# Performance work log

Hardware: AMD Instinct MI355X
Metric: run time of the kernel (lower is better)

## Reference

```python
import jax, jax.numpy as jnp
import numpy as np

HIDDEN = 1024
FFN = 2048
NUM_EXPERTS = 8
TOP_K = 2
BATCH, SEQ = 2, 1024


def setup_inputs() -> dict:
    key = jax.random.key(0)
    k0, k1, k2, k3, k4 = jax.random.split(key, 5)
    scale = 0.02
    hidden_states = jax.random.normal(k0, (BATCH, SEQ, HIDDEN), dtype=jnp.float32)
    gate_w = jax.random.normal(k1, (NUM_EXPERTS, HIDDEN), dtype=jnp.float32) * scale
    w1 = jax.random.normal(k2, (NUM_EXPERTS, FFN, HIDDEN), dtype=jnp.float32) * scale  # gate proj
    w3 = jax.random.normal(k3, (NUM_EXPERTS, FFN, HIDDEN), dtype=jnp.float32) * scale  # up proj
    w2 = jax.random.normal(k4, (NUM_EXPERTS, HIDDEN, FFN), dtype=jnp.float32) * scale  # down proj
    return {"hidden_states": hidden_states, "gate_w": gate_w, "w1": w1, "w2": w2, "w3": w3}


def reference(hidden_states, gate_w, w1, w2, w3):
    B, S, D = hidden_states.shape
    x = hidden_states.reshape(-1, D)                         # [T, D]
    T = x.shape[0]
    # Router: logits -> fp32 softmax -> top-k -> renormalize
    router_logits = jnp.einsum("td,ed->te", x, gate_w)       # [T, E]
    routing_weights = jax.nn.softmax(router_logits.astype(jnp.float32), axis=1)
    top_vals, top_idx = jax.lax.top_k(routing_weights, TOP_K)  # [T, K]
    top_vals = top_vals / jnp.sum(top_vals, axis=-1, keepdims=True)
    top_vals = top_vals.astype(x.dtype)
    # Per-token-per-expert combine weight (0 for unselected experts)
    w_te = jnp.zeros((T, NUM_EXPERTS), dtype=x.dtype)
    w_te = w_te.at[jnp.arange(T)[:, None], top_idx].add(top_vals)  # [T, E]
    # Fused experts: silu(x W1^T) * (x W3^T) -> W2^T, weighted combine
    g = jax.nn.silu(jnp.einsum("td,efd->tef", x, w1))        # [T, E, F]
    u = jnp.einsum("td,efd->tef", x, w3)                     # [T, E, F]
    y = jnp.einsum("tef,edf->ted", g * u, w2)                # [T, E, D]
    out = jnp.einsum("ted,te->td", y, w_te)                  # [T, D]
    return out.reshape(B, S, D), router_logits
```

## Files before the change

### kernel.cpp

```cpp
#include <hip/hip_runtime.h>
#include <hip/hip_bf16.h>
#include <stdint.h>

#define HIDDEN  1024
#define FFN_DIM 2048
#define NEXP    8
#define NTOK    2048
#define MAXROWS 5120

typedef short bf16x8 __attribute__((ext_vector_type(8)));
typedef float f32x4  __attribute__((ext_vector_type(4)));

static const size_t OFF_CNT  = 0;
static const size_t OFF_BASE = 64;
static const size_t OFF_TOK  = 128;
static const size_t OFF_WGT  = OFF_TOK + (size_t)NEXP*NTOK*4;
static const size_t OFF_XBF  = 131328;
static const size_t XBF_B    = (size_t)NTOK*HIDDEN*2;
static const size_t OFF_W1B  = OFF_XBF + XBF_B;
static const size_t W_B      = (size_t)NEXP*FFN_DIM*HIDDEN*2;
static const size_t OFF_W3B  = OFF_W1B + W_B;
static const size_t OFF_W2B  = OFF_W3B + W_B;
static const size_t OFF_H    = OFF_W2B + W_B;
static const size_t H_B      = (size_t)MAXROWS*FFN_DIM*2;
static const size_t WS_NEED  = OFF_H + H_B;

__device__ __forceinline__ unsigned short f2bf(float f) {
  union { float f; unsigned u; } a; a.f = f;
  unsigned r = a.u + 0x7fff + ((a.u >> 16) & 1);
  return (unsigned short)(r >> 16);
}

__device__ __forceinline__ void ld_g2l16(const void* gsrc, void* ldst) {
  __builtin_amdgcn_global_load_lds(
      (const __attribute__((address_space(1))) unsigned int*)gsrc,
      (__attribute__((address_space(3))) unsigned int*)ldst, 16, 0, 0);
}

__global__ __launch_bounds__(256) void router_kernel(
    const float* __restrict__ x, const float* __restrict__ gw,
    float* __restrict__ logits, int* __restrict__ cnt,
    int* __restrict__ tok, float* __restrict__ wgt)
{
  const int t   = blockIdx.x;
  const int tid = threadIdx.x;
  float4 xv = ((const float4*)(x + (size_t)t * HIDDEN))[tid];
  float p[NEXP];
#pragma unroll
  for (int e = 0; e < NEXP; ++e) {
    float4 gv = ((const float4*)(gw + (size_t)e * HIDDEN))[tid];
    p[e] = xv.x * gv.x + xv.y * gv.y + xv.z * gv.z + xv.w * gv.w;
  }
#pragma unroll
  for (int e = 0; e < NEXP; ++e) {
#pragma unroll
    for (int off = 32; off > 0; off >>= 1)
      p[e] += __shfl_down(p[e], off, 64);
  }
  __shared__ float red[4][NEXP];
  const int wv = tid >> 6, ln = tid & 63;
  if (ln == 0) {
#pragma unroll
    for (int e = 0; e < NEXP; ++e) red[wv][e] = p[e];
  }
  __syncthreads();
  if (tid == 0) {
    float l[NEXP];
#pragma unroll
    for (int e = 0; e < NEXP; ++e) {
      l[e] = red[0][e] + red[1][e] + red[2][e] + red[3][e];
      logits[(size_t)t * NEXP + e] = l[e];
    }
    int i0 = 0;
#pragma unroll
    for (int e = 1; e < NEXP; ++e) if (l[e] > l[i0]) i0 = e;
    int i1 = (i0 == 0) ? 1 : 0;
#pragma unroll
    for (int e = 0; e < NEXP; ++e) if (e != i0 && l[e] > l[i1]) i1 = e;
    float w0 = 1.f / (1.f + expf(l[i1] - l[i0]));
    float w1 = 1.f - w0;
    int s0 = atomicAdd(&cnt[i0], 1);
    tok[i0 * NTOK + s0] = t;  wgt[i0 * NTOK + s0] = w0;
    int s1 = atomicAdd(&cnt[i1], 1);
    tok[i1 * NTOK + s1] = t;  wgt[i1 * NTOK + s1] = w1;
  }
}

__global__ void prefix_kernel(const int* __restrict__ cnt, int* __restrict__ base) {
  if (threadIdx.x == 0 && blockIdx.x == 0) {
    int b = 0;
#pragma unroll
    for (int e = 0; e < NEXP; ++e) { base[e] = b; b += ((cnt[e] + 127) >> 7) << 7; }
    base[NEXP] = b;
  }
}

__global__ __launch_bounds__(256) void cvt_kernel(
    const float* __restrict__ src, unsigned short* __restrict__ dst, int n4)
{
  int i = blockIdx.x * blockDim.x + threadIdx.x;
  const int stride = gridDim.x * blockDim.x;
  for (; i < n4; i += stride) {
    float4 v = ((const float4*)src)[i];
    ushort4 o;
    o.x = f2bf(v.x); o.y = f2bf(v.y); o.z = f2bf(v.z); o.w = f2bf(v.w);
    ((ushort4*)dst)[i] = o;
  }
}

__global__ __launch_bounds__(256) void cvt3_kernel(
    const float* __restrict__ s0, const float* __restrict__ s1, const float* __restrict__ s2,
    unsigned short* __restrict__ d0, unsigned short* __restrict__ d1, unsigned short* __restrict__ d2,
    int n4)
{
  const int start  = blockIdx.x * blockDim.x + threadIdx.x;
  const int stride = gridDim.x * blockDim.x;
#pragma unroll
  for (int pass = 0; pass < 3; ++pass) {
    const float* s = (pass == 0) ? s0 : (pass == 1) ? s1 : s2;
    unsigned short* d = (pass == 0) ? d0 : (pass == 1) ? d1 : d2;
    for (int i = start; i < n4; i += stride) {
      float4 v = ((const float4*)s)[i];
      ushort4 o;
      o.x = f2bf(v.x); o.y = f2bf(v.y); o.z = f2bf(v.z); o.w = f2bf(v.w);
      ((ushort4*)d)[i] = o;
    }
  }
}

__global__ __launch_bounds__(512) void gemm1_kernel(
    const unsigned short* __restrict__ xbf,
    const unsigned short* __restrict__ w1bf,
    const unsigned short* __restrict__ w3bf,
    const int* __restrict__ cnt, const int* __restrict__ base,
    const int* __restrict__ tok,
    unsigned short* __restrict__ H)
{
  const int bid  = blockIdx.x;
  const int e    = bid & 7;
  const int slot = bid >> 3;
  const int mt   = slot & 15;
  const int nt   = slot >> 4;
  const int n = cnt[e];
  if (mt * 128 >= n) return;
  const int t = threadIdx.x;
  const int w = t >> 6, l = t & 63;

  __shared__ unsigned short Xs [128 * 64];
  __shared__ unsigned short W1s[128 * 64];
  __shared__ unsigned short W3s[128 * 64];
  __shared__ int stok[128];

  if (t < 128) {
    int idx = mt * 128 + t;
    stok[t] = tok[e * NTOK + min(idx, n - 1)];
  }
  __syncthreads();

  const int r0 = t >> 3;
  const size_t tok0 = (size_t)stok[r0];
  const size_t tok1 = (size_t)stok[64 + r0];
  const int kp = (((t & 7) ^ ((t >> 3) & 7)) << 3);

  const unsigned short* w1e = w1bf + (size_t)e * FFN_DIM * HIDDEN + (size_t)(nt * 128) * HIDDEN;
  const unsigned short* w3e = w3bf + (size_t)e * FFN_DIM * HIDDEN + (size_t)(nt * 128) * HIDDEN;

  f32x4 acc1[4][2], acc3[4][2];
#pragma unroll
  for (int i = 0; i < 4; ++i)
#pragma unroll
    for (int j = 0; j < 2; ++j) { acc1[i][j] = (f32x4)0.f; acc3[i][j] = (f32x4)0.f; }

  const int Moff = (w & 1) * 64;
  const int Noff = (w >> 1) * 32;
  const int lr = l & 15;
  const int lg = l >> 4;
  char* ldsX = (char*)Xs  + w * 1024;
  char* ldsA = (char*)W1s + w * 1024;
  char* ldsB = (char*)W3s + w * 1024;

  for (int kb = 0; kb < HIDDEN / 64; ++kb) {
    __syncthreads();
    const int kofs = kb * 64 + kp;
    ld_g2l16(xbf + tok0 * HIDDEN + kofs,               ldsX);
    ld_g2l16(xbf + tok1 * HIDDEN + kofs,               ldsX + 8192);
    ld_g2l16(w1e + (size_t)r0 * HIDDEN + kofs,         ldsA);
    ld_g2l16(w1e + (size_t)(64 + r0) * HIDDEN + kofs,  ldsA + 8192);
    ld_g2l16(w3e + (size_t)r0 * HIDDEN + kofs,         ldsB);
    ld_g2l16(w3e + (size_t)(64 + r0) * HIDDEN + kofs,  ldsB + 8192);
    __syncthreads();
#pragma unroll
    for (int s = 0; s < 2; ++s) {
      const int ug = 4 * s + lg;
      bf16x8 a[4], b1[2], b3[2];
#pragma unroll
      for (int mi = 0; mi < 4; ++mi) {
        const int R = Moff + mi * 16 + lr;
        a[mi] = *(const bf16x8*)&Xs[R * 64 + ((ug ^ (lr & 7)) << 3)];
      }
#pragma unroll
      for (int ni = 0; ni < 2; ++ni) {
        const int R = Noff + ni * 16 + lr;
        b1[ni] = *(const bf16x8*)&W1s[R * 64 + ((ug ^ (lr & 7)) << 3)];
        b3[ni] = *(const bf16x8*)&W3s[R * 64 + ((ug ^ (lr & 7)) << 3)];
      }
#pragma unroll
      for (int mi = 0; mi < 4; ++mi)
#pragma unroll
        for (int ni = 0; ni < 2; ++ni) {
          acc1[mi][ni] = __builtin_amdgcn_mfma_f32_16x16x32_bf16(a[mi], b1[ni], acc1[mi][ni], 0, 0, 0);
          acc3[mi][ni] = __builtin_amdgcn_mfma_f32_16x16x32_bf16(a[mi], b3[ni], acc3[mi][ni], 0, 0, 0);
        }
    }
  }

  const size_t rbase = (size_t)base[e] + (size_t)mt * 128;
#pragma unroll
  for (int mi = 0; mi < 4; ++mi)
#pragma unroll
    for (int ni = 0; ni < 2; ++ni)
#pragma unroll
      for (int j = 0; j < 4; ++j) {
        int row = Moff + mi * 16 + lg * 4 + j;
        int col = nt * 128 + Noff + ni * 16 + lr;
        float s1 = acc1[mi][ni][j], s3 = acc3[mi][ni][j];
        float h = (s1 / (1.f + __expf(-s1))) * s3;
        H[(rbase + row) * FFN_DIM + col] = f2bf(h);
      }
}

__global__ __launch_bounds__(512) void gemm2_kernel(
    const unsigned short* __restrict__ H,
    const unsigned short* __restrict__ w2bf,
    const int* __restrict__ cnt, const int* __restrict__ base,
    const int* __restrict__ tok, const float* __restrict__ wgt,
    float* __restrict__ out)
{
  const int bid  = blockIdx.x;
  const int e    = bid & 7;
  const int slot = bid >> 3;
  const int mt   = slot & 15;
  const int nt   = slot >> 4;
  const int n = cnt[e];
  if (mt * 128 >= n) return;
  const int t = threadIdx.x;
  const int w = t >> 6, l = t & 63;

  __shared__ unsigned short Hs[128 * 64];
  __shared__ unsigned short Ws[128 * 64];
  __shared__ int   stok[128];
  __shared__ float swgt[128];

  if (t < 128) {
    int idx = mt * 128 + t;
    int ok = idx < n;
    stok[t] = ok ? tok[e * NTOK + idx] : -1;
    swgt[t] = ok ? wgt[e * NTOK + idx] : 0.f;
  }

  const int r0 = t >> 3;
  const int kp = (((t & 7) ^ ((t >> 3) & 7)) << 3);
  const unsigned short* He  = H + (size_t)(base[e] + mt * 128) * FFN_DIM;
  const unsigned short* w2e = w2bf + (size_t)e * HIDDEN * FFN_DIM + (size_t)(nt * 128) * FFN_DIM;

  f32x4 acc[4][2];
#pragma unroll
  for (int i = 0; i < 4; ++i)
#pragma unroll
    for (int j = 0; j < 2; ++j) acc[i][j] = (f32x4)0.f;

  const int Moff = (w & 1) * 64;
  const int Noff = (w >> 1) * 32;
  const int lr = l & 15;
  const int lg = l >> 4;
  char* ldsH = (char*)Hs + w * 1024;
  char* ldsW = (char*)Ws + w * 1024;

  for (int kb = 0; kb < FFN_DIM / 64; ++kb) {
    __syncthreads();
    const int kofs = kb * 64 + kp;
    ld_g2l16(He  + (size_t)r0 * FFN_DIM + kofs,        ldsH);
    ld_g2l16(He  + (size_t)(64 + r0) * FFN_DIM + kofs, ldsH + 8192);
    ld_g2l16(w2e + (size_t)r0 * FFN_DIM + kofs,        ldsW);
    ld_g2l16(w2e + (size_t)(64 + r0) * FFN_DIM + kofs, ldsW + 8192);
    __syncthreads();
#pragma unroll
    for (int s = 0; s < 2; ++s) {
      const int ug = 4 * s + lg;
      bf16x8 a[4], b[2];
#pragma unroll
      for (int mi = 0; mi < 4; ++mi) {
        const int R = Moff + mi * 16 + lr;
        a[mi] = *(const bf16x8*)&Hs[R * 64 + ((ug ^ (lr & 7)) << 3)];
      }
#pragma unroll
      for (int ni = 0; ni < 2; ++ni) {
        const int R = Noff + ni * 16 + lr;
        b[ni] = *(const bf16x8*)&Ws[R * 64 + ((ug ^ (lr & 7)) << 3)];
      }
#pragma unroll
      for (int mi = 0; mi < 4; ++mi)
#pragma unroll
        for (int ni = 0; ni < 2; ++ni)
          acc[mi][ni] = __builtin_amdgcn_mfma_f32_16x16x32_bf16(a[mi], b[ni], acc[mi][ni], 0, 0, 0);
    }
  }

#pragma unroll
  for (int mi = 0; mi < 4; ++mi)
#pragma unroll
    for (int ni = 0; ni < 2; ++ni)
#pragma unroll
      for (int j = 0; j < 4; ++j) {
        int row = Moff + mi * 16 + lg * 4 + j;
        int tk = stok[row];
        if (tk >= 0) {
          int col = nt * 128 + Noff + ni * 16 + lr;
          atomicAdd(&out[(size_t)tk * HIDDEN + col], swgt[row] * acc[mi][ni][j]);
        }
      }
}

#define TT 12
#define FC 256
#define NCHUNK (FFN_DIM / FC)

__global__ __launch_bounds__(256) void moe_ffn_kernel(
    const float* __restrict__ x,
    const float* __restrict__ w1, const float* __restrict__ w2,
    const float* __restrict__ w3,
    const int* __restrict__ cnt, const int* __restrict__ tok,
    const float* __restrict__ wgt, float* __restrict__ out)
{
  const int e  = blockIdx.y;
  const int n  = cnt[e];
  const int ts = blockIdx.x * TT;
  if (ts >= n) return;
  const int tid = threadIdx.x;

  __shared__ float xs[TT * HIDDEN];
  __shared__ float hc[TT * FC];
  __shared__ int   stok[TT];
  __shared__ float swgt[TT];

  if (tid < TT) {
    int idx = ts + tid;
    int tk  = (idx < n) ? tok[e * NTOK + idx] : -1;
    stok[tid] = tk;
    swgt[tid] = (idx < n) ? wgt[e * NTOK + idx] : 0.f;
  }
  __syncthreads();
#pragma unroll
  for (int i = 0; i < TT; ++i) {
    int tk = stok[i];
    float4 v = make_float4(0.f, 0.f, 0.f, 0.f);
    if (tk >= 0) v = ((const float4*)(x + (size_t)tk * HIDDEN))[tid];
    ((float4*)(xs + i * HIDDEN))[tid] = v;
  }
  __syncthreads();

  const float* w1e = w1 + (size_t)e * FFN_DIM * HIDDEN;
  const float* w3e = w3 + (size_t)e * FFN_DIM * HIDDEN;
  const float* w2e = w2 + (size_t)e * HIDDEN * FFN_DIM;

  float yacc[4][TT];
#pragma unroll
  for (int j = 0; j < 4; ++j)
#pragma unroll
    for (int t = 0; t < TT; ++t) yacc[j][t] = 0.f;

  for (int c = 0; c < NCHUNK; ++c) {
    const int f = c * FC + tid;
    const float4* r1 = (const float4*)(w1e + (size_t)f * HIDDEN);
    const float4* r3 = (const float4*)(w3e + (size_t)f * HIDDEN);
    float a1[TT], a3[TT];
#pragma unroll
    for (int t = 0; t < TT; ++t) { a1[t] = 0.f; a3[t] = 0.f; }
    for (int k = 0; k < HIDDEN / 4; ++k) {
      float4 v1 = r1[k];
      float4 v3 = r3[k];
#pragma unroll
      for (int t = 0; t < TT; ++t) {
        float4 xv = *(const float4*)(xs + t * HIDDEN + 4 * k);
        a1[t] += xv.x * v1.x + xv.y * v1.y + xv.z * v1.z + xv.w * v1.w;
        a3[t] += xv.x * v3.x + xv.y * v3.y + xv.z * v3.z + xv.w * v3.w;
      }
    }
    __syncthreads();
#pragma unroll
    for (int t = 0; t < TT; ++t) {
      float g  = a1[t];
      float sg = g / (1.f + __expf(-g));
      hc[t * FC + tid] = sg * a3[t];
    }
    __syncthreads();
    const float4* r20 = (const float4*)(w2e + (size_t)(tid      ) * FFN_DIM + c * FC);
    const float4* r21 = (const float4*)(w2e + (size_t)(tid + 256) * FFN_DIM + c * FC);
    const float4* r22 = (const float4*)(w2e + (size_t)(tid + 512) * FFN_DIM + c * FC);
    const float4* r23 = (const float4*)(w2e + (size_t)(tid + 768) * FFN_DIM + c * FC);
    for (int k = 0; k < FC / 4; ++k) {
      float4 wv0 = r20[k], wv1 = r21[k], wv2 = r22[k], wv3 = r23[k];
#pragma unroll
      for (int t = 0; t < TT; ++t) {
        float4 hv = *(const float4*)(hc + t * FC + 4 * k);
        yacc[0][t] += hv.x * wv0.x + hv.y * wv0.y + hv.z * wv0.z + hv.w * wv0.w;
        yacc[1][t] += hv.x * wv1.x + hv.y * wv1.y + hv.z * wv1.z + hv.w * wv1.w;
        yacc[2][t] += hv.x * wv2.x + hv.y * wv2.y + hv.z * wv2.z + hv.w * wv2.w;
        yacc[3][t] += hv.x * wv3.x + hv.y * wv3.y + hv.z * wv3.z + hv.w * wv3.w;
      }
    }
  }

#pragma unroll
  for (int t = 0; t < TT; ++t) {
    int tk = stok[t];
    if (tk < 0) continue;
    float wt = swgt[t];
    float* orow = out + (size_t)tk * HIDDEN;
    atomicAdd(orow + tid,       wt * yacc[0][t]);
    atomicAdd(orow + tid + 256, wt * yacc[1][t]);
    atomicAdd(orow + tid + 512, wt * yacc[2][t]);
    atomicAdd(orow + tid + 768, wt * yacc[3][t]);
  }
}

extern "C" void kernel_launch(void* const* d_in, const int* in_sizes, int n_in,
                              void* d_out, int out_size, void* d_ws, size_t ws_size,
                              hipStream_t stream) {
  const float* x  = (const float*)d_in[0];
  const float* gw = (const float*)d_in[1];
  const float* w1 = (const float*)d_in[2];
  const float* w2 = (const float*)d_in[3];
  const float* w3 = (const float*)d_in[4];
  float* out    = (float*)d_out;
  float* logits = out + (size_t)NTOK * HIDDEN;

  char* ws = (char*)d_ws;
  int*   cnt  = (int*)(ws + OFF_CNT);
  int*   base = (int*)(ws + OFF_BASE);
  int*   tokp = (int*)(ws + OFF_TOK);
  float* wgtp = (float*)(ws + OFF_WGT);

  hipMemsetAsync(out, 0, (size_t)NTOK * HIDDEN * sizeof(float), stream);
  hipMemsetAsync(cnt, 0, NEXP * sizeof(int), stream);

  router_kernel<<<NTOK, 256, 0, stream>>>(x, gw, logits, cnt, tokp, wgtp);

  if (ws_size >= WS_NEED) {
    unsigned short* xbf  = (unsigned short*)(ws + OFF_XBF);
    unsigned short* w1bf = (unsigned short*)(ws + OFF_W1B);
    unsigned short* w3bf = (unsigned short*)(ws + OFF_W3B);
    unsigned short* w2bf = (unsigned short*)(ws + OFF_W2B);
    unsigned short* Hbuf = (unsigned short*)(ws + OFF_H);

    cvt_kernel<<<256, 256, 0, stream>>>(x, xbf, (int)(NTOK * HIDDEN / 4));
    cvt3_kernel<<<2048, 256, 0, stream>>>(w1, w3, w2, w1bf, w3bf, w2bf,
                                          (int)(NEXP * FFN_DIM * HIDDEN / 4));

    prefix_kernel<<<1, 64, 0, stream>>>(cnt, base);

    gemm1_kernel<<<NEXP * 16 * 16, 512, 0, stream>>>(xbf, w1bf, w3bf, cnt, base, tokp, Hbuf);
    gemm2_kernel<<<NEXP * 16 * 8, 512, 0, stream>>>(Hbuf, w2bf, cnt, base, tokp, wgtp, out);
  } else {
    dim3 grid((NTOK + TT - 1) / TT, NEXP);
    moe_ffn_kernel<<<grid, 256, 0, stream>>>(x, w1, w2, w3, cnt, tokp, wgtp, out);
  }
}
```

Baseline: 218.3 us.

## Fuse fp32-to-bf16 weight conversion into expert GEMM tile loads

Removes the separate pass that converted all expert weights to bf16 in a workspace. The GEMM kernels now read fp32 weights directly, convert them in registers with the packed bf16 convert instruction, and store them to LDS. This drops a full read-write pass over 200MB of weights and the bf16 workspace, but each weight tile is now re-read in fp32 (twice the bytes) by every token tile that touches it, and register-staged loads replace the async global-to-LDS path. It also adds launch_bounds occupancy hints.

```diff
diff --git a/kernel.cpp b/kernel.cpp
--- a/kernel.cpp
+++ b/kernel.cpp
@@ -17,11 +17,7 @@
 static const size_t OFF_WGT  = OFF_TOK + (size_t)NEXP*NTOK*4;
 static const size_t OFF_XBF  = 131328;
 static const size_t XBF_B    = (size_t)NTOK*HIDDEN*2;
-static const size_t OFF_W1B  = OFF_XBF + XBF_B;
-static const size_t W_B      = (size_t)NEXP*FFN_DIM*HIDDEN*2;
-static const size_t OFF_W3B  = OFF_W1B + W_B;
-static const size_t OFF_W2B  = OFF_W3B + W_B;
-static const size_t OFF_H    = OFF_W2B + W_B;
+static const size_t OFF_H    = OFF_XBF + XBF_B;
 static const size_t H_B      = (size_t)MAXROWS*FFN_DIM*2;
 static const size_t WS_NEED  = OFF_H + H_B;
 
@@ -29,6 +25,15 @@
   union { float f; unsigned u; } a; a.f = f;
   unsigned r = a.u + 0x7fff + ((a.u >> 16) & 1);
   return (unsigned short)(r >> 16);
+}
+
+__device__ __forceinline__ uint4 cvt8(float4 a, float4 b) {
+  uint4 r;
+  asm("v_cvt_pk_bf16_f32 %0, %1, %2" : "=v"(r.x) : "v"(a.x), "v"(a.y));
+  asm("v_cvt_pk_bf16_f32 %0, %1, %2" : "=v"(r.y) : "v"(a.z), "v"(a.w));
+  asm("v_cvt_pk_bf16_f32 %0, %1, %2" : "=v"(r.z) : "v"(b.x), "v"(b.y));
+  asm("v_cvt_pk_bf16_f32 %0, %1, %2" : "=v"(r.w) : "v"(b.z), "v"(b.w));
+  return r;
 }
 
 __device__ __forceinline__ void ld_g2l16(const void* gsrc, void* ldst) {
@@ -108,30 +113,10 @@
   }
 }
 
-__global__ __launch_bounds__(256) void cvt3_kernel(
-    const float* __restrict__ s0, const float* __restrict__ s1, const float* __restrict__ s2,
-    unsigned short* __restrict__ d0, unsigned short* __restrict__ d1, unsigned short* __restrict__ d2,
-    int n4)
-{
-  const int start  = blockIdx.x * blockDim.x + threadIdx.x;
-  const int stride = gridDim.x * blockDim.x;
-#pragma unroll
-  for (int pass = 0; pass < 3; ++pass) {
-    const float* s = (pass == 0) ? s0 : (pass == 1) ? s1 : s2;
-    unsigned short* d = (pass == 0) ? d0 : (pass == 1) ? d1 : d2;
-    for (int i = start; i < n4; i += stride) {
-      float4 v = ((const float4*)s)[i];
-      ushort4 o;
-      o.x = f2bf(v.x); o.y = f2bf(v.y); o.z = f2bf(v.z); o.w = f2bf(v.w);
-      ((ushort4*)d)[i] = o;
-    }
-  }
-}
-
-__global__ __launch_bounds__(512) void gemm1_kernel(
+__global__ __launch_bounds__(512, 4) void gemm1_kernel(
     const unsigned short* __restrict__ xbf,
-    const unsigned short* __restrict__ w1bf,
-    const unsigned short* __restrict__ w3bf,
+    const float* __restrict__ w1f,
+    const float* __restrict__ w3f,
     const int* __restrict__ cnt, const int* __restrict__ base,
     const int* __restrict__ tok,
     unsigned short* __restrict__ H)
@@ -162,8 +147,18 @@
   const size_t tok1 = (size_t)stok[64 + r0];
   const int kp = (((t & 7) ^ ((t >> 3) & 7)) << 3);
 
-  const unsigned short* w1e = w1bf + (size_t)e * FFN_DIM * HIDDEN + (size_t)(nt * 128) * HIDDEN;
-  const unsigned short* w3e = w3bf + (size_t)e * FFN_DIM * HIDDEN + (size_t)(nt * 128) * HIDDEN;
+  const float* w1e = w1f + (size_t)e * FFN_DIM * HIDDEN + (size_t)(nt * 128) * HIDDEN;
+  const float* w3e = w3f + (size_t)e * FFN_DIM * HIDDEN + (size_t)(nt * 128) * HIDDEN;
+  const float* w1p0 = w1e + (size_t)r0        * HIDDEN + kp;
+  const float* w1p1 = w1e + (size_t)(64 + r0) * HIDDEN + kp;
+  const float* w3p0 = w3e + (size_t)r0        * HIDDEN + kp;
+  const float* w3p1 = w3e + (size_t)(64 + r0) * HIDDEN + kp;
+
+  uint4* lw1a = (uint4*)((char*)W1s + t * 16);
+  uint4* lw1b = (uint4*)((char*)W1s + 8192 + t * 16);
+  uint4* lw3a = (uint4*)((char*)W3s + t * 16);
+  uint4* lw3b = (uint4*)((char*)W3s + 8192 + t * 16);
+  char* ldsX = (char*)Xs + w * 1024;
 
   f32x4 acc1[4][2], acc3[4][2];
 #pragma unroll
@@ -175,24 +170,32 @@
   const int Noff = (w >> 1) * 32;
   const int lr = l & 15;
   const int lg = l >> 4;
-  char* ldsX = (char*)Xs  + w * 1024;
-  char* ldsA = (char*)W1s + w * 1024;
-  char* ldsB = (char*)W3s + w * 1024;
 
   for (int kb = 0; kb < HIDDEN / 64; ++kb) {
     __syncthreads();
     const int kofs = kb * 64 + kp;
-    ld_g2l16(xbf + tok0 * HIDDEN + kofs,               ldsX);
-    ld_g2l16(xbf + tok1 * HIDDEN + kofs,               ldsX + 8192);
-    ld_g2l16(w1e + (size_t)r0 * HIDDEN + kofs,         ldsA);
-    ld_g2l16(w1e + (size_t)(64 + r0) * HIDDEN + kofs,  ldsA + 8192);
-    ld_g2l16(w3e + (size_t)r0 * HIDDEN + kofs,         ldsB);
-    ld_g2l16(w3e + (size_t)(64 + r0) * HIDDEN + kofs,  ldsB + 8192);
+    ld_g2l16(xbf + tok0 * HIDDEN + kofs, ldsX);
+    ld_g2l16(xbf + tok1 * HIDDEN + kofs, ldsX + 8192);
+    {
+      const int ko = kb * 64;
+      float4 a0 = *(const float4*)(w1p0 + ko);
+      float4 a1 = *(const float4*)(w1p0 + ko + 4);
+      float4 a2 = *(const float4*)(w1p1 + ko);
+      float4 a3 = *(const float4*)(w1p1 + ko + 4);
+      float4 b0 = *(const float4*)(w3p0 + ko);
+      float4 b1 = *(const float4*)(w3p0 + ko + 4);
+      float4 b2 = *(const float4*)(w3p1 + ko);
+      float4 b3 = *(const float4*)(w3p1 + ko + 4);
+      *lw1a = cvt8(a0, a1);
+      *lw1b = cvt8(a2, a3);
+      *lw3a = cvt8(b0, b1);
+      *lw3b = cvt8(b2, b3);
+    }
     __syncthreads();
 #pragma unroll
     for (int s = 0; s < 2; ++s) {
       const int ug = 4 * s + lg;
-      bf16x8 a[4], b1[2], b3[2];
+      bf16x8 a[4], b1v[2], b3v[2];
 #pragma unroll
       for (int mi = 0; mi < 4; ++mi) {
         const int R = Moff + mi * 16 + lr;
@@ -201,15 +204,15 @@
 #pragma unroll
       for (int ni = 0; ni < 2; ++ni) {
         const int R = Noff + ni * 16 + lr;
-        b1[ni] = *(const bf16x8*)&W1s[R * 64 + ((ug ^ (lr & 7)) << 3)];
-        b3[ni] = *(const bf16x8*)&W3s[R * 64 + ((ug ^ (lr & 7)) << 3)];
+        b1v[ni] = *(const bf16x8*)&W1s[R * 64 + ((ug ^ (lr & 7)) << 3)];
+        b3v[ni] = *(const bf16x8*)&W3s[R * 64 + ((ug ^ (lr & 7)) << 3)];
       }
 #pragma unroll
       for (int mi = 0; mi < 4; ++mi)
 #pragma unroll
         for (int ni = 0; ni < 2; ++ni) {
-          acc1[mi][ni] = __builtin_amdgcn_mfma_f32_16x16x32_bf16(a[mi], b1[ni], acc1[mi][ni], 0, 0, 0);
-          acc3[mi][ni] = __builtin_amdgcn_mfma_f32_16x16x32_bf16(a[mi], b3[ni], acc3[mi][ni], 0, 0, 0);
+          acc1[mi][ni] = __builtin_amdgcn_mfma_f32_16x16x32_bf16(a[mi], b1v[ni], acc1[mi][ni], 0, 0, 0);
+          acc3[mi][ni] = __builtin_amdgcn_mfma_f32_16x16x32_bf16(a[mi], b3v[ni], acc3[mi][ni], 0, 0, 0);
         }
     }
   }
@@ -229,9 +232,9 @@
       }
 }
 
-__global__ __launch_bounds__(512) void gemm2_kernel(
+__global__ __launch_bounds__(512, 4) void gemm2_kernel(
     const unsigned short* __restrict__ H,
-    const unsigned short* __restrict__ w2bf,
+    const float* __restrict__ w2f,
     const int* __restrict__ cnt, const int* __restrict__ base,
     const int* __restrict__ tok, const float* __restrict__ wgt,
     float* __restrict__ out)
@@ -260,8 +263,14 @@
 
   const int r0 = t >> 3;
   const int kp = (((t & 7) ^ ((t >> 3) & 7)) << 3);
-  const unsigned short* He  = H + (size_t)(base[e] + mt * 128) * FFN_DIM;
-  const unsigned short* w2e = w2bf + (size_t)e * HIDDEN * FFN_DIM + (size_t)(nt * 128) * FFN_DIM;
+  const unsigned short* He = H + (size_t)(base[e] + mt * 128) * FFN_DIM;
+  const float* w2e  = w2f + (size_t)e * HIDDEN * FFN_DIM + (size_t)(nt * 128) * FFN_DIM;
+  const float* w2p0 = w2e + (size_t)r0        * FFN_DIM + kp;
+  const float* w2p1 = w2e + (size_t)(64 + r0) * FFN_DIM + kp;
+
+  uint4* lwa = (uint4*)((char*)Ws + t * 16);
+  uint4* lwb = (uint4*)((char*)Ws + 8192 + t * 16);
+  char* ldsH = (char*)Hs + w * 1024;
 
   f32x4 acc[4][2];
 #pragma unroll
@@ -273,16 +282,21 @@
   const int Noff = (w >> 1) * 32;
   const int lr = l & 15;
   const int lg = l >> 4;
-  char* ldsH = (char*)Hs + w * 1024;
-  char* ldsW = (char*)Ws + w * 1024;
 
   for (int kb = 0; kb < FFN_DIM / 64; ++kb) {
     __syncthreads();
     const int kofs = kb * 64 + kp;
-    ld_g2l16(He  + (size_t)r0 * FFN_DIM + kofs,        ldsH);
-    ld_g2l16(He  + (size_t)(64 + r0) * FFN_DIM + kofs, ldsH + 8192);
-    ld_g2l16(w2e + (size_t)r0 * FFN_DIM + kofs,        ldsW);
-    ld_g2l16(w2e + (size_t)(64 + r0) * FFN_DIM + kofs, ldsW + 8192);
+    ld_g2l16(He + (size_t)r0 * FFN_DIM + kofs,        ldsH);
+    ld_g2l16(He + (size_t)(64 + r0) * FFN_DIM + kofs, ldsH + 8192);
+    {
+      const int ko = kb * 64;
+      float4 a0 = *(const float4*)(w2p0 + ko);
+      float4 a1 = *(const float4*)(w2p0 + ko + 4);
+      float4 a2 = *(const float4*)(w2p1 + ko);
+      float4 a3 = *(const float4*)(w2p1 + ko + 4);
+      *lwa = cvt8(a0, a1);
+      *lwb = cvt8(a2, a3);
+    }
     __syncthreads();
 #pragma unroll
     for (int s = 0; s < 2; ++s) {
@@ -448,19 +462,13 @@
 
   if (ws_size >= WS_NEED) {
     unsigned short* xbf  = (unsigned short*)(ws + OFF_XBF);
-    unsigned short* w1bf = (unsigned short*)(ws + OFF_W1B);
-    unsigned short* w3bf = (unsigned short*)(ws + OFF_W3B);
-    unsigned short* w2bf = (unsigned short*)(ws + OFF_W2B);
     unsigned short* Hbuf = (unsigned short*)(ws + OFF_H);
 
-    cvt_kernel<<<256, 256, 0, stream>>>(x, xbf, (int)(NTOK * HIDDEN / 4));
-    cvt3_kernel<<<2048, 256, 0, stream>>>(w1, w3, w2, w1bf, w3bf, w2bf,
-                                          (int)(NEXP * FFN_DIM * HIDDEN / 4));
-
+    cvt_kernel<<<512, 256, 0, stream>>>(x, xbf, (int)(NTOK * HIDDEN / 4));
     prefix_kernel<<<1, 64, 0, stream>>>(cnt, base);
 
-    gemm1_kernel<<<NEXP * 16 * 16, 512, 0, stream>>>(xbf, w1bf, w3bf, cnt, base, tokp, Hbuf);
-    gemm2_kernel<<<NEXP * 16 * 8, 512, 0, stream>>>(Hbuf, w2bf, cnt, base, tokp, wgtp, out);
+    gemm1_kernel<<<NEXP * 16 * 16, 512, 0, stream>>>(xbf, w1, w3, cnt, base, tokp, Hbuf);
+    gemm2_kernel<<<NEXP * 16 * 8, 512, 0, stream>>>(Hbuf, w2, cnt, base, tokp, wgtp, out);
   } else {
     dim3 grid((NTOK + TT - 1) / TT, NEXP);
     moe_ffn_kernel<<<grid, 256, 0, stream>>>(x, w1, w2, w3, cnt, tokp, wgtp, out);
```

Result: slower. 227.1 us (+4.0%).
